# Performance work log

Hardware: AMD Instinct MI355X
Metric: run time of the kernel (lower is better)

## Reference

```python
import jax, jax.numpy as jnp
import numpy as np

B, H, E, V = 128, 1024, 1024, 40000
L, S, A = 256, 10, 10
L_S, L_A = 1.0, 1.0  # s_copy_lambda / a_copy_lambda
NEG = -1e24


def setup_inputs():
    key = jax.random.key(0)
    ks = jax.random.split(key, 32)
    n = lambda i, shape: jax.random.normal(ks[i], shape, dtype=jnp.float32)
    p = lambda i, shape: jax.random.normal(ks[i], shape, dtype=jnp.float32) * 0.02
    rnn_in = 3 * E + H  # embed + history ctx (H) + state ctx (E) + action ctx (E)
    return {
        "inp": n(0, (B, 1, E)),
        "hidden": n(1, (1, B, H)),
        "hs_vectors": n(2, (B, L, H)),
        "state_gumbel_prob": jax.random.uniform(ks[3], (B, S, V), dtype=jnp.float32),
        "state_gumbel_embed": n(4, (B, S, E)),
        "action_gumbel_prob": jax.random.uniform(ks[5], (B, A, V), dtype=jnp.float32),
        "action_gumbel_embed": n(6, (B, A, E)),
        "history_lens": jax.random.randint(ks[7], (B,), 1, L + 1),
        "history_word_indices": jax.random.randint(ks[8], (B, L), 0, V),
        # history word mlp-attention
        "Wq_hist": p(9, (H, H)), "bq_hist": jnp.zeros((H,), jnp.float32),
        "Wm_hist": p(10, (H, H)), "v_hist": p(11, (H,)),
        # init_s_attn / init_a_attn (query H, memory E)
        "Wq_s": p(12, (H, H)), "bq_s": jnp.zeros((H,), jnp.float32),
        "Wm_s": p(13, (E, H)), "v_s": p(14, (H,)),
        "Wq_a": p(15, (H, H)), "bq_a": jnp.zeros((H,), jnp.float32),
        "Wm_a": p(16, (E, H)), "v_a": p(17, (H,)),
        # sparse_copy_attn (memory E+1)
        "Wq_sc": p(18, (H, H)), "bq_sc": jnp.zeros((H,), jnp.float32),
        "Wm_sc": p(19, (E + 1, H)), "v_sc": p(20, (H,)),
        # GRU (torch layout: [3H, in], gate order r,z,n)
        "W_ih": p(21, (3 * H, rnn_in)), "W_hh": p(22, (3 * H, H)),
        "b_ih": jnp.zeros((3 * H,), jnp.float32), "b_hh": jnp.zeros((3 * H,), jnp.float32),
        # output projection
        "W_out": p(23, (H, V)), "b_out": jnp.zeros((V,), jnp.float32),
    }


def _mlp_scores(q, mem, Wq, bq, Wm, v):
    # q: [B,1,H], mem: [B,L,M] -> additive-attention logits [B,1,L]
    t = jnp.tanh((q @ Wq + bq) + (mem @ Wm))  # [B,L,H]
    return (t @ v)[:, None, :]


def reference(inp, hidden, hs_vectors, state_gumbel_prob, state_gumbel_embed,
              action_gumbel_prob, action_gumbel_embed, history_lens,
              history_word_indices, Wq_hist, bq_hist, Wm_hist, v_hist,
              Wq_s, bq_s, Wm_s, v_s, Wq_a, bq_a, Wm_a, v_a,
              Wq_sc, bq_sc, Wm_sc, v_sc, W_ih, W_hh, b_ih, b_hh, W_out, b_out):
    q0 = jnp.transpose(hidden, (1, 0, 2))  # [B,1,H]
    # --- history word attention (masked mlp attention) ---
    hist_scores = _mlp_scores(q0, hs_vectors, Wq_hist, bq_hist, Wm_hist, v_hist)
    valid = jnp.arange(L)[None, None, :] < history_lens[:, None, None]
    hist_scores = jnp.where(valid, hist_scores, NEG)
    c_his = jax.nn.softmax(hist_scores, axis=-1) @ hs_vectors  # [B,1,H]
    # --- init_consult over state / action gumbel embeddings ---
    sw = jax.nn.softmax(_mlp_scores(q0, state_gumbel_embed, Wq_s, bq_s, Wm_s, v_s), axis=-1)
    c_state = sw @ state_gumbel_embed  # [B,1,E]
    aw = jax.nn.softmax(_mlp_scores(q0, action_gumbel_embed, Wq_a, bq_a, Wm_a, v_a), axis=-1)
    c_action = aw @ action_gumbel_embed  # [B,1,E]
    x = jnp.concatenate([inp, c_his, c_state, c_action], axis=-1)[:, 0, :]  # [B,3E+H]
    # --- single-step GRU cell (torch semantics, gate order r,z,n) ---
    h0 = hidden[0]
    gi = x @ W_ih.T + b_ih
    gh = h0 @ W_hh.T + b_hh
    ir, iz, inn = jnp.split(gi, 3, axis=-1)
    hr, hz, hn = jnp.split(gh, 3, axis=-1)
    r = jax.nn.sigmoid(ir + hr)
    z = jax.nn.sigmoid(iz + hz)
    nact = jnp.tanh(inn + r * hn)
    h_new = (1.0 - z) * nact + z * h0  # [B,H]
    # --- vocab logits + copy logits, joint softmax ---
    gene_logits = h_new @ W_out + b_out  # [B,V]
    cq = h_new[:, None, :]
    hs_logits = jnp.einsum('bqh,blh->bql', cq, hs_vectors)[:, 0, :]  # dot attn, [B,L]
    s_tag = jnp.zeros((B, S, 1), jnp.float32)
    a_tag = jnp.ones((B, A, 1), jnp.float32)
    st_logits = _mlp_scores(cq, jnp.concatenate([state_gumbel_embed, s_tag], -1), Wq_sc, bq_sc, Wm_sc, v_sc)[:, 0, :]
    ac_logits = _mlp_scores(cq, jnp.concatenate([action_gumbel_embed, a_tag], -1), Wq_sc, bq_sc, Wm_sc, v_sc)[:, 0, :]
    all_logits = jnp.concatenate([gene_logits, hs_logits, st_logits, ac_logits], axis=-1)
    wp = jax.nn.softmax(all_logits, axis=-1)  # [B, V+L+S+A]
    gene_p = wp[:, :V]
    hs_w = wp[:, V:V + L]
    st_w = wp[:, V + L:V + L + S]
    ac_w = wp[:, V + L + S:]
    # --- copy-distribution mixing ---
    scp = jnp.einsum('bs,bsv->bv', st_w, state_gumbel_prob)
    acp = jnp.einsum('ba,bav->bv', ac_w, action_gumbel_prob)
    gene_p = gene_p + L_S * scp + L_A * acp
    copy_p = jnp.zeros((B, V), jnp.float32).at[jnp.arange(B)[:, None], history_word_indices].add(hs_w)
    out = jnp.log(gene_p + copy_p)[:, None, :]  # [B,1,V]
    return out, h_new[None]
```

## Files before the change

### kernel.cpp

```cpp
#include <hip/hip_runtime.h>
#include <stdint.h>

typedef __attribute__((ext_vector_type(4))) float f32x4;
typedef __attribute__((ext_vector_type(2))) unsigned int u32x2;
typedef __attribute__((ext_vector_type(4))) unsigned int u32x4;
typedef __attribute__((ext_vector_type(8))) short bf16x8;

#define BV (128*40000)

__device__ __forceinline__ unsigned rne_bf16(float f) {
    unsigned x = __float_as_uint(f);
    return ((x + 0x7FFFu + ((x >> 16) & 1u)) >> 16) & 0xFFFFu;
}
__device__ __forceinline__ unsigned pack2(float a, float b) {
    return rne_bf16(a) | (rne_bf16(b) << 16);
}
__device__ __forceinline__ float bf2f(unsigned u) {
    return __uint_as_float((u & 0xFFFFu) << 16);
}
__device__ __forceinline__ float sigm(float x) { return 1.0f / (1.0f + expf(-x)); }
__device__ __forceinline__ float ftanh(float x) {
    float e = __expf(2.0f * x);
    return 1.0f - 2.0f / (e + 1.0f);
}

__device__ __forceinline__ void gload16(const void* g, void* l) {
    __builtin_amdgcn_global_load_lds(
        (const __attribute__((address_space(1))) unsigned*)g,
        (__attribute__((address_space(3))) unsigned*)l, 16, 0, 0);
}

struct BigArgs {
    const unsigned short *hs, *WmhT, *se, *ae, *WmsT, *WmaT;
    const int* lens;
    const float *qh_h, *bq_h, *v_h;
    const float *qh_s, *bq_s, *v_s;
    const float *qh_a, *bq_a, *v_a;
    float *hsc, *stsc, *acsc;
};

__global__ __launch_bounds__(512, 1) void k_big(BigArgs a, int* __restrict__ ctr) {
    __shared__ unsigned short As[2][16384];
    __shared__ unsigned short Bs[2][16384];
    __shared__ int sTile;

    const int t = threadIdx.x, lane = t & 63, wv = t >> 6;
    const int l16 = lane & 15, lq = lane >> 4;
    const int wm = wv >> 2, wn = wv & 3;

    const int srowL = t >> 3;
    const int gccA = ((t & 7) ^ (srowL & 7)) << 3;
    const int sw = l16 & 7;
    const int c0 = ((lq ^ sw) << 3);
    const int A0 = (wm << 13) + (l16 << 6);
    const int B0 = ((wn >> 1) << 13) + ((((wn & 1) << 6) + l16) << 6);

#define STAGE(kt, d)                                                          \
    {                                                                         \
        const unsigned short* ga_ = gA + (size_t)(kt) * 64;                   \
        const unsigned short* gb_ = gB + (size_t)(kt) * 64;                   \
        _Pragma("unroll")                                                     \
        for (int h_ = 0; h_ < 2; ++h_) {                                      \
            _Pragma("unroll")                                                 \
            for (int r_ = 0; r_ < 2; ++r_) {                                  \
                size_t go_ = (size_t)(h_ * 128 + r_ * 64) * 1024;             \
                int lo_ = h_ * 8192 + r_ * 4096 + (wv << 9);                  \
                gload16(ga_ + go_, &As[d][lo_]);                              \
                gload16(gb_ + go_, &Bs[d][lo_]);                              \
            }                                                                 \
        }                                                                     \
    }

    for (;;) {
        __syncthreads();
        if (t == 0) sTile = atomicAdd(ctr, 1);
        __syncthreads();
        const int wg = sTile;
        if (wg >= 552) return;

        const unsigned short *A, *Bt;
        const float *rb, *cb, *vv;
        float* out;
        int m0, n0, vrows, rpb;
        if (wg < 40) {
            int op = wg / 20, r = wg - op * 20;
            int mt = r >> 2, nt = r & 3;
            if (op == 0) { A = a.se; Bt = a.WmsT; rb = a.qh_s; cb = a.bq_s; vv = a.v_s; out = a.stsc; }
            else         { A = a.ae; Bt = a.WmaT; rb = a.qh_a; cb = a.bq_a; vv = a.v_a; out = a.acsc; }
            m0 = mt << 8; n0 = nt << 8; vrows = 256; rpb = 10;
        } else {
            int h = wg - 40;
            int m = h >> 2, n = h & 3;
            A = a.hs; Bt = a.WmhT; rb = a.qh_h; cb = a.bq_h; vv = a.v_h; out = a.hsc;
            m0 = m << 8; n0 = n << 8; vrows = a.lens[m]; rpb = 256;
        }

        const unsigned short* gA = A + (size_t)(m0 + srowL) * 1024 + gccA;
        const unsigned short* gB = Bt + (size_t)(n0 + srowL) * 1024 + gccA;

        f32x4 acc[8][4];
#pragma unroll
        for (int i = 0; i < 8; ++i)
#pragma unroll
            for (int j = 0; j < 4; ++j) acc[i][j] = (f32x4){0.f, 0.f, 0.f, 0.f};

        STAGE(0, 0);
        for (int kt = 0; kt < 16; ++kt) {
            int cur = kt & 1;
            if (kt < 15) {
                STAGE(kt + 1, cur ^ 1);
                asm volatile("s_waitcnt vmcnt(8)" ::: "memory");
            } else {
                asm volatile("s_waitcnt vmcnt(0)" ::: "memory");
            }
            __builtin_amdgcn_s_barrier();
            __builtin_amdgcn_sched_barrier(0);

            const unsigned short* ab = As[cur];
            const unsigned short* bb = Bs[cur];
            if (vrows > (wm << 7)) {
                bf16x8 bf0[4], bf1[4];
#pragma unroll
                for (int nf = 0; nf < 4; ++nf) {
                    bf0[nf] = *(const bf16x8*)(bb + B0 + (nf << 10) + c0);
                    bf1[nf] = *(const bf16x8*)(bb + B0 + (nf << 10) + (c0 ^ 32));
                }
#pragma unroll
                for (int mf = 0; mf < 8; ++mf) {
                    if ((wm << 7) + (mf << 4) < vrows) {
                        bf16x8 a0 = *(const bf16x8*)(ab + A0 + (mf << 10) + c0);
                        bf16x8 a1 = *(const bf16x8*)(ab + A0 + (mf << 10) + (c0 ^ 32));
#pragma unroll
                        for (int nf = 0; nf < 4; ++nf)
                            acc[mf][nf] = __builtin_amdgcn_mfma_f32_16x16x32_bf16(a0, bf0[nf], acc[mf][nf], 0, 0, 0);
#pragma unroll
                        for (int nf = 0; nf < 4; ++nf)
                            acc[mf][nf] = __builtin_amdgcn_mfma_f32_16x16x32_bf16(a1, bf1[nf], acc[mf][nf], 0, 0, 0);
                    }
                }
            }
            __builtin_amdgcn_sched_barrier(0);
            __builtin_amdgcn_s_barrier();
        }

        float cbv[4], vvv[4];
        int gcs[4];
#pragma unroll
        for (int nf = 0; nf < 4; ++nf) {
            int gc = n0 + (wn << 6) + (nf << 4) + l16;
            gcs[nf] = gc; cbv[nf] = cb[gc]; vvv[nf] = vv[gc];
        }
#pragma unroll
        for (int mf = 0; mf < 8; ++mf) {
            int rloc = (wm << 7) + (mf << 4);
            if (rloc < vrows) {
#pragma unroll
                for (int r = 0; r < 4; ++r) {
                    int gr = m0 + rloc + (lq << 2) + r;
                    const float* rbp = rb + (size_t)(gr / rpb) * 1024;
                    float s = 0.f;
#pragma unroll
                    for (int nf = 0; nf < 4; ++nf) {
                        float x = acc[mf][nf][r] + rbp[gcs[nf]] + cbv[nf];
                        s += ftanh(x) * vvv[nf];
                    }
#pragma unroll
                    for (int m2 = 1; m2 < 16; m2 <<= 1) s += __shfl_xor(s, m2, 64);
                    if (l16 == 0) atomicAdd(&out[gr], s);
                }
            }
        }
    }
#undef STAGE
}

template<int EPI>
__device__ __forceinline__ void mgemm(
    const unsigned short* __restrict__ A, const unsigned short* __restrict__ Bt,
    float* __restrict__ out, const float* __restrict__ rb,
    const float* __restrict__ cb1, const float* __restrict__ cb2,
    const float* __restrict__ vvec,
    int m0, int n0, int kb, int ke, int ldk, int ldc, int rpb)
{
    __shared__ unsigned short As[2][4096];
    __shared__ unsigned short Bs[2][4096];
    const int t = threadIdx.x, lane = t & 63, wv = t >> 6;
    const int l16 = lane & 15, lq = lane >> 4;
    const int wm = wv >> 1, wn = wv & 1;

    const int srow = lane >> 2, scol = (lane & 3) << 3;
    const unsigned short* gA0 = A + (size_t)(m0 + (wv << 4) + srow) * ldk + kb + scol;
    const unsigned short* gA1 = gA0 + (size_t)64 * ldk;
    const unsigned short* gB0 = Bt + (size_t)(n0 + (wv << 4) + srow) * ldk + kb + scol;
    const unsigned short* gB1 = gB0 + (size_t)64 * ldk;
    unsigned short* lA0 = &As[0][wv << 9];
    unsigned short* lA1 = &As[0][(wv + 4) << 9];
    unsigned short* lB0 = &Bs[0][wv << 9];
    unsigned short* lB1 = &Bs[0][(wv + 4) << 9];

    f32x4 acc[4][4];
#pragma unroll
    for (int i = 0; i < 4; ++i)
#pragma unroll
        for (int j = 0; j < 4; ++j) acc[i][j] = (f32x4){0.f, 0.f, 0.f, 0.f};

    const int NS = (ke - kb) >> 5;
    gload16(gA0, lA0); gload16(gA1, lA1);
    gload16(gB0, lB0); gload16(gB1, lB1);

    for (int s = 0; s < NS; ++s) {
        __syncthreads();
        if (s + 1 < NS) {
            const int nb = (s + 1) & 1, ko = (s + 1) << 5;
            gload16(gA0 + ko, lA0 + (nb << 12)); gload16(gA1 + ko, lA1 + (nb << 12));
            gload16(gB0 + ko, lB0 + (nb << 12)); gload16(gB1 + ko, lB1 + (nb << 12));
        }
        const unsigned short* ab = As[s & 1];
        const unsigned short* bb = Bs[s & 1];
        bf16x8 af[4], bfv[4];
#pragma unroll
        for (int i = 0; i < 4; ++i)
            af[i] = *(const bf16x8*)(ab + (((wm << 6) + (i << 4) + l16) << 5) + (lq << 3));
#pragma unroll
        for (int i = 0; i < 4; ++i)
            bfv[i] = *(const bf16x8*)(bb + (((wn << 6) + (i << 4) + l16) << 5) + (lq << 3));
#pragma unroll
        for (int mf = 0; mf < 4; ++mf)
#pragma unroll
            for (int nf = 0; nf < 4; ++nf)
                acc[mf][nf] = __builtin_amdgcn_mfma_f32_16x16x32_bf16(af[mf], bfv[nf], acc[mf][nf], 0, 0, 0);
    }

    if (EPI == 1) {
#pragma unroll
        for (int mf = 0; mf < 4; ++mf) {
#pragma unroll
            for (int r = 0; r < 4; ++r) {
                int gr = m0 + (wm << 6) + (mf << 4) + (lq << 2) + r;
                const float* rbp = rb + (size_t)(gr / rpb) * 1024;
                float s = 0.0f;
#pragma unroll
                for (int nf = 0; nf < 4; ++nf) {
                    int gc = n0 + (wn << 6) + (nf << 4) + l16;
                    float xv = acc[mf][nf][r] + rbp[gc] + cb1[gc];
                    if (cb2) xv += cb2[gc];
                    s += ftanh(xv) * vvec[gc];
                }
#pragma unroll
                for (int msk = 1; msk < 16; msk <<= 1) s += __shfl_xor(s, msk, 64);
                if (l16 == 0) atomicAdd(&out[gr], s);
            }
        }
    } else {
#pragma unroll
        for (int mf = 0; mf < 4; ++mf) {
            int gr0 = m0 + (wm << 6) + (mf << 4) + (lq << 2);
#pragma unroll
            for (int nf = 0; nf < 4; ++nf) {
                int gc = n0 + (wn << 6) + (nf << 4) + l16;
#pragma unroll
                for (int r = 0; r < 4; ++r)
                    atomicAdd(&out[(size_t)(gr0 + r) * ldc + gc], acc[mf][nf][r]);
            }
        }
    }
}

__device__ __forceinline__ void gene_body(
    const unsigned short* __restrict__ hnb, const float* __restrict__ Wout,
    const float* __restrict__ b_out, float* __restrict__ out, int n0)
{
    __shared__ unsigned short As[2][4096];
    __shared__ unsigned short Bs[2][4096];
    const int t = threadIdx.x, lane = t & 63, wv = t >> 6;
    const int l16 = lane & 15, lq = lane >> 4;
    const int wm = wv >> 1, wn = wv & 1;

    const int srow = lane >> 2, scol = (lane & 3) << 3;
    const unsigned short* gA0 = hnb + (size_t)((wv << 4) + srow) * 1024 + scol;
    const unsigned short* gA1 = gA0 + (size_t)64 * 1024;
    unsigned short* lA0 = &As[0][wv << 9];
    unsigned short* lA1 = &As[0][(wv + 4) << 9];

    const int bn = t & 127, kh = t >> 7;
    const bool ok = (n0 + bn) < 40000;
    const float* gB = Wout + (size_t)(kh * 16) * 40000 + (n0 + bn);

    f32x4 acc[4][4];
#pragma unroll
    for (int i = 0; i < 4; ++i)
#pragma unroll
        for (int j = 0; j < 4; ++j) acc[i][j] = (f32x4){0.f, 0.f, 0.f, 0.f};

    auto stageB = [&](int buf, int ko) {
        const float* src = gB + (size_t)ko * 40000;
        float f[16];
#pragma unroll
        for (int j = 0; j < 16; ++j) f[j] = ok ? src[(size_t)j * 40000] : 0.0f;
        u32x4* d = (u32x4*)&Bs[buf][bn * 32 + kh * 16];
        d[0] = (u32x4){pack2(f[0],f[1]), pack2(f[2],f[3]), pack2(f[4],f[5]), pack2(f[6],f[7])};
        d[1] = (u32x4){pack2(f[8],f[9]), pack2(f[10],f[11]), pack2(f[12],f[13]), pack2(f[14],f[15])};
    };

    gload16(gA0, lA0); gload16(gA1, lA1); stageB(0, 0);
    for (int s = 0; s < 32; ++s) {
        __syncthreads();
        if (s + 1 < 32) {
            const int nb = (s + 1) & 1, ko = (s + 1) << 5;
            gload16(gA0 + ko, lA0 + (nb << 12)); gload16(gA1 + ko, lA1 + (nb << 12));
            stageB(nb, ko);
        }
        const unsigned short* ab = As[s & 1];
        const unsigned short* bb = Bs[s & 1];
        bf16x8 af[4], bfv[4];
#pragma unroll
        for (int i = 0; i < 4; ++i)
            af[i] = *(const bf16x8*)(ab + (((wm << 6) + (i << 4) + l16) << 5) + (lq << 3));
#pragma unroll
        for (int i = 0; i < 4; ++i)
            bfv[i] = *(const bf16x8*)(bb + (((wn << 6) + (i << 4) + l16) << 5) + (lq << 3));
#pragma unroll
        for (int mf = 0; mf < 4; ++mf)
#pragma unroll
            for (int nf = 0; nf < 4; ++nf)
                acc[mf][nf] = __builtin_amdgcn_mfma_f32_16x16x32_bf16(af[mf], bfv[nf], acc[mf][nf], 0, 0, 0);
    }
#pragma unroll
    for (int mf = 0; mf < 4; ++mf) {
        int gr0 = (wm << 6) + (mf << 4) + (lq << 2);
#pragma unroll
        for (int nf = 0; nf < 4; ++nf) {
            int gc = n0 + (wn << 6) + (nf << 4) + l16;
            if (gc < 40000) {
                float bo = b_out[gc];
#pragma unroll
                for (int r = 0; r < 4; ++r)
                    out[(size_t)(gr0 + r) * 40000 + gc] = acc[mf][nf][r] + bo;
            }
        }
    }
}

__global__ __launch_bounds__(256) void k_stac3(
    const unsigned short* se, const unsigned short* ae, const unsigned short* WmscT,
    const float* tagrow, const float* qsc, const float* bq_sc, const float* v_sc,
    float* stlg, float* aclg) {
    if (blockIdx.z == 0)
        mgemm<1>(se, WmscT, stlg, qsc, bq_sc, nullptr, v_sc, blockIdx.y * 128, blockIdx.x * 128, 0, 1024, 1024, 0, 10);
    else
        mgemm<1>(ae, WmscT, aclg, qsc, bq_sc, tagrow, v_sc, blockIdx.y * 128, blockIdx.x * 128, 0, 1024, 1024, 0, 10);
}

__global__ __launch_bounds__(256) void k_qh4(
    const unsigned short* q0, const unsigned short* W0, const unsigned short* W1,
    const unsigned short* W2, float* o0, float* o1, float* o2) {
    const unsigned short* W = W0; float* o = o0;
    if (blockIdx.z == 1) { W = W1; o = o1; }
    if (blockIdx.z == 2) { W = W2; o = o2; }
    int kb = blockIdx.y << 8;
    mgemm<2>(q0, W, o, nullptr, nullptr, nullptr, nullptr, 0, blockIdx.x * 128, kb, kb + 256, 1024, 1024, 1);
}

__global__ __launch_bounds__(256) void k_gigh2(
    const unsigned short* xb, const unsigned short* q0,
    const unsigned short* Wih, const unsigned short* Whh, float* gi, float* gh) {
    if (blockIdx.z == 0) {
        int kb = blockIdx.y << 9;
        mgemm<2>(xb, Wih, gi, nullptr, nullptr, nullptr, nullptr, 0, blockIdx.x * 128, kb, kb + 512, 4096, 3072, 1);
    } else {
        if (blockIdx.y >= 2) return;
        int kb = blockIdx.y << 9;
        mgemm<2>(q0, Whh, gh, nullptr, nullptr, nullptr, nullptr, 0, blockIdx.x * 128, kb, kb + 512, 1024, 3072, 1);
    }
}

__global__ __launch_bounds__(256) void k_qsc_gene(
    const unsigned short* hnb, const unsigned short* WqscT, float* qsc,
    const float* Wout, const float* b_out, float* out) {
    int id = blockIdx.x;
    if (id < 16) {
        int x = id & 7, kb = (id >> 3) << 9;
        mgemm<2>(hnb, WqscT, qsc, nullptr, nullptr, nullptr, nullptr, 0, x * 128, kb, kb + 512, 1024, 1024, 1);
    } else {
        gene_body(hnb, Wout, b_out, out, (id - 16) << 7);
    }
}

struct CvtArgs { const float* s[6]; unsigned short* d[6]; int pre[7]; };
__global__ __launch_bounds__(256) void k_cvt_all(CvtArgs a) {
    int total = a.pre[6];
    for (int i = blockIdx.x * 256 + threadIdx.x; i < total; i += gridDim.x * 256) {
        int seg = 0;
        while (i >= a.pre[seg + 1]) ++seg;
        int loc = i - a.pre[seg];
        const f32x4* s4 = (const f32x4*)a.s[seg] + (size_t)loc * 2;
        f32x4 q0 = s4[0], q1 = s4[1];
        ((u32x4*)a.d[seg])[loc] =
            (u32x4){pack2(q0[0],q0[1]), pack2(q0[2],q0[3]), pack2(q1[0],q1[1]), pack2(q1[2],q1[3])};
    }
}

struct TrArgs { const float* s[8]; unsigned short* d[8]; };
__global__ __launch_bounds__(256) void k_trcvt(TrArgs a) {
    __shared__ float tile[64][65];
    const float* in = a.s[blockIdx.z];
    unsigned short* ot = a.d[blockIdx.z];
    int k0 = blockIdx.y << 6, n0 = blockIdx.x << 6;
    int tr = threadIdx.x >> 6, tc = threadIdx.x & 63;
#pragma unroll
    for (int i = 0; i < 16; ++i) {
        int r = (i << 2) + tr;
        tile[r][tc] = in[(size_t)(k0 + r) * 1024 + n0 + tc];
    }
    __syncthreads();
#pragma unroll
    for (int i = 0; i < 16; ++i) {
        int r = (i << 2) + tr;
        ot[(size_t)(n0 + r) * 1024 + k0 + tc] = (unsigned short)rne_bf16(tile[tc][r]);
    }
}

__device__ __forceinline__ void softmax10(const float* src, float* dst) {
    float m = src[0];
    for (int i = 1; i < 10; ++i) m = fmaxf(m, src[i]);
    float z = 0.f, e[10];
    for (int i = 0; i < 10; ++i) { e[i] = expf(src[i] - m); z += e[i]; }
    float iz = 1.0f / z;
    for (int i = 0; i < 10; ++i) dst[i] = e[i] * iz;
}

__global__ __launch_bounds__(256) void k_ctx(
    const float* __restrict__ scores, const int* __restrict__ lens,
    const unsigned short* __restrict__ hs,
    const float* __restrict__ inp, const float* __restrict__ st_sc, const float* __restrict__ ac_sc,
    const unsigned short* __restrict__ se, const unsigned short* __restrict__ ae,
    unsigned short* __restrict__ xb) {
    int b = blockIdx.x, t = threadIdx.x;
    __shared__ float w[256];
    __shared__ float red[256];
    __shared__ float sw[10], aw[10];
    int len = lens[b];
    float s = scores[b * 256 + t];
    bool valid = t < len;
    red[t] = valid ? s : -3.0e38f;
    __syncthreads();
    for (int st = 128; st > 0; st >>= 1) { if (t < st) red[t] = fmaxf(red[t], red[t + st]); __syncthreads(); }
    float m = red[0];
    __syncthreads();
    float e = valid ? expf(s - m) : 0.0f;
    red[t] = e;
    __syncthreads();
    for (int st = 128; st > 0; st >>= 1) { if (t < st) red[t] += red[t + st]; __syncthreads(); }
    float Z = red[0];
    __syncthreads();
    w[t] = e / Z;
    if (t == 0) softmax10(st_sc + b * 10, sw);
    if (t == 64) softmax10(ac_sc + b * 10, aw);
    f32x4 iv = ((const f32x4*)(inp + (size_t)b * 1024))[t];
    *((u32x2*)(xb + (size_t)b * 4096) + t) = (u32x2){pack2(iv[0], iv[1]), pack2(iv[2], iv[3])};
    __syncthreads();
    float a0 = 0.f, a1 = 0.f, a2 = 0.f, a3 = 0.f;
    for (int l = 0; l < 256; ++l) {
        float wl = w[l];
        if (wl == 0.0f) continue;
        u32x2 u = *((const u32x2*)(hs + ((size_t)b * 256 + l) * 1024) + t);
        a0 += wl * bf2f(u[0]); a1 += wl * bf2f(u[0] >> 16);
        a2 += wl * bf2f(u[1]); a3 += wl * bf2f(u[1] >> 16);
    }
    *((u32x2*)(xb + (size_t)b * 4096 + 1024) + t) = (u32x2){pack2(a0, a1), pack2(a2, a3)};
    float cs0=0,cs1=0,cs2=0,cs3=0, ca0=0,ca1=0,ca2=0,ca3=0;
#pragma unroll
    for (int q = 0; q < 10; ++q) {
        u32x2 us = *((const u32x2*)(se + ((size_t)b * 10 + q) * 1024) + t);
        u32x2 ua = *((const u32x2*)(ae + ((size_t)b * 10 + q) * 1024) + t);
        float ws = sw[q], wa = aw[q];
        cs0 += ws * bf2f(us[0]); cs1 += ws * bf2f(us[0] >> 16);
        cs2 += ws * bf2f(us[1]); cs3 += ws * bf2f(us[1] >> 16);
        ca0 += wa * bf2f(ua[0]); ca1 += wa * bf2f(ua[0] >> 16);
        ca2 += wa * bf2f(ua[1]); ca3 += wa * bf2f(ua[1] >> 16);
    }
    *((u32x2*)(xb + (size_t)b * 4096 + 2048) + t) = (u32x2){pack2(cs0, cs1), pack2(cs2, cs3)};
    *((u32x2*)(xb + (size_t)b * 4096 + 3072) + t) = (u32x2){pack2(ca0, ca1), pack2(ca2, ca3)};
}

__global__ __launch_bounds__(1024) void k_gruhsl(
    const float* __restrict__ gi, const float* __restrict__ gh,
    const float* __restrict__ b_ih, const float* __restrict__ b_hh,
    const float* __restrict__ h0, float* __restrict__ hnew,
    unsigned short* __restrict__ hnb,
    const unsigned short* __restrict__ hs, float* __restrict__ hsl) {
    int b = blockIdx.x, j = threadIdx.x;
    size_t i = (size_t)b * 1024 + j;
    const float* gib = gi + (size_t)b * 3072;
    const float* ghb = gh + (size_t)b * 3072;
    float r = sigm(gib[j] + b_ih[j] + ghb[j] + b_hh[j]);
    float z = sigm(gib[1024 + j] + b_ih[1024 + j] + ghb[1024 + j] + b_hh[1024 + j]);
    float hn = ghb[2048 + j] + b_hh[2048 + j];
    float n = tanhf(gib[2048 + j] + b_ih[2048 + j] + r * hn);
    float h = (1.0f - z) * n + z * h0[i];
    hnew[i] = h;
    hnb[i] = (unsigned short)rne_bf16(h);
    __shared__ float hsm[1024];
    hsm[j] = h;
    __syncthreads();
    int wave = j >> 6, lane = j & 63;
    float hr[16];
#pragma unroll
    for (int k = 0; k < 16; ++k) hr[k] = hsm[lane * 16 + k];
    for (int l = wave; l < 256; l += 16) {
        const u32x4* row = (const u32x4*)(hs + ((size_t)b * 256 + l) * 1024);
        u32x4 u0 = row[lane * 2], u1 = row[lane * 2 + 1];
        float s = hr[0]*bf2f(u0[0]) + hr[1]*bf2f(u0[0]>>16) + hr[2]*bf2f(u0[1]) + hr[3]*bf2f(u0[1]>>16)
                + hr[4]*bf2f(u0[2]) + hr[5]*bf2f(u0[2]>>16) + hr[6]*bf2f(u0[3]) + hr[7]*bf2f(u0[3]>>16)
                + hr[8]*bf2f(u1[0]) + hr[9]*bf2f(u1[0]>>16) + hr[10]*bf2f(u1[1]) + hr[11]*bf2f(u1[1]>>16)
                + hr[12]*bf2f(u1[2]) + hr[13]*bf2f(u1[2]>>16) + hr[14]*bf2f(u1[3]) + hr[15]*bf2f(u1[3]>>16);
#pragma unroll
        for (int msk = 1; msk < 64; msk <<= 1) s += __shfl_xor(s, msk, 64);
        if (lane == 0) hsl[b * 256 + l] = s;
    }
}

__global__ __launch_bounds__(256) void k_smsc(
    const float* __restrict__ gene, const float* __restrict__ hsl,
    const float* __restrict__ stl, const float* __restrict__ acl,
    const int* __restrict__ hwi,
    float* __restrict__ mbuf, float* __restrict__ zbuf, float* __restrict__ copyp) {
    int b = blockIdx.x, t = threadIdx.x;
    __shared__ float red[256];
    const f32x4* g4 = (const f32x4*)(gene + (size_t)b * 40000);
    float mx = -3.0e38f;
    for (int i = t; i < 10000; i += 256) {
        f32x4 q = g4[i];
        mx = fmaxf(mx, fmaxf(fmaxf(q[0], q[1]), fmaxf(q[2], q[3])));
    }
    float hv = hsl[b * 256 + t];
    mx = fmaxf(mx, hv);
    if (t < 10) mx = fmaxf(mx, fmaxf(stl[b * 10 + t], acl[b * 10 + t]));
    red[t] = mx; __syncthreads();
    for (int s = 128; s > 0; s >>= 1) { if (t < s) red[t] = fmaxf(red[t], red[t + s]); __syncthreads(); }
    float m = red[0];
    __syncthreads();
    float sum = 0.f;
    for (int i = t; i < 10000; i += 256) {
        f32x4 q = g4[i];
        sum += expf(q[0]-m) + expf(q[1]-m) + expf(q[2]-m) + expf(q[3]-m);
    }
    sum += expf(hv - m);
    if (t < 10) sum += expf(stl[b * 10 + t] - m) + expf(acl[b * 10 + t] - m);
    red[t] = sum; __syncthreads();
    for (int s = 128; s > 0; s >>= 1) { if (t < s) red[t] += red[t + s]; __syncthreads(); }
    float Z = red[0];
    if (t == 0) { mbuf[b] = m; zbuf[b] = Z; }
    float wv = expf(hv - m) / Z;
    atomicAdd(copyp + (size_t)b * 40000 + hwi[b * 256 + t], wv);
}

__global__ __launch_bounds__(256) void k_final(
    float* __restrict__ gene_out, const float* __restrict__ copyp,
    const float* __restrict__ sprob, const float* __restrict__ aprob,
    const float* __restrict__ stl, const float* __restrict__ acl,
    const float* __restrict__ mbuf, const float* __restrict__ zbuf) {
    int b = blockIdx.y, t = threadIdx.x;
    __shared__ float sw[10], aw[10];
    float m = mbuf[b], iz = 1.0f / zbuf[b];
    if (t < 10) sw[t] = expf(stl[b * 10 + t] - m) * iz;
    if (t >= 64 && t < 74) aw[t - 64] = expf(acl[b * 10 + (t - 64)] - m) * iz;
    __syncthreads();
    int v4 = blockIdx.x * 256 + t;
    if (v4 < 10000) {
        size_t base = (size_t)b * 10000 + v4;
        f32x4 g = ((const f32x4*)gene_out)[base];
        f32x4 c = ((const f32x4*)copyp)[base];
        f32x4 acc;
#pragma unroll
        for (int j = 0; j < 4; ++j) acc[j] = expf(g[j] - m) * iz + c[j];
#pragma unroll
        for (int s = 0; s < 10; ++s) {
            f32x4 pv = ((const f32x4*)sprob)[((size_t)b * 10 + s) * 10000 + v4];
            f32x4 av = ((const f32x4*)aprob)[((size_t)b * 10 + s) * 10000 + v4];
            float ws = sw[s], wa = aw[s];
#pragma unroll
            for (int j = 0; j < 4; ++j) acc[j] += ws * pv[j] + wa * av[j];
        }
        f32x4 r;
#pragma unroll
        for (int j = 0; j < 4; ++j) r[j] = logf(acc[j]);
        ((f32x4*)gene_out)[base] = r;
    }
}

#define OFF_QH_H  0
#define OFF_QH_S  131072
#define OFF_QH_A  262144
#define OFF_QSC   393216
#define OFF_GI    524288
#define OFF_GH    917504
#define OFF_HSC   1310720
#define OFF_STSC  1343488
#define OFF_ACSC  1344768
#define OFF_STLG  1346048
#define OFF_ACLG  1347328
#define OFF_CTR   1348608
#define ZERO_FLOATS 1348736
#define OFF_HSL   1348736
#define OFF_M     1381504
#define OFF_Z     1381632
#define OFF_COPY  1381760
#define FLOAT_TOTAL 6501760
#define SO_HS     0
#define SO_SE     33554432
#define SO_AE     34865152
#define SO_Q0     36175872
#define SO_X      36306944
#define SO_HNB    36831232
#define SO_WQHT   36962304
#define SO_WQST   38010880
#define SO_WQAT   39059456
#define SO_WQSCT  40108032
#define SO_WMHT   41156608
#define SO_WMST   42205184
#define SO_WMAT   43253760
#define SO_WMSCT  44302336
#define SO_WIH    45350912
#define SO_WHH    57933824

extern "C" void kernel_launch(void* const* d_in, const int* in_sizes, int n_in,
                              void* d_out, int out_size, void* d_ws, size_t ws_size,
                              hipStream_t stream) {
    const float* inp     = (const float*)d_in[0];
    const float* hidden  = (const float*)d_in[1];
    const float* hs      = (const float*)d_in[2];
    const float* sprob   = (const float*)d_in[3];
    const float* se      = (const float*)d_in[4];
    const float* aprob   = (const float*)d_in[5];
    const float* ae      = (const float*)d_in[6];
    const int*   lens    = (const int*)d_in[7];
    const int*   hwi     = (const int*)d_in[8];
    const float* Wq_hist = (const float*)d_in[9];
    const float* bq_hist = (const float*)d_in[10];
    const float* Wm_hist = (const float*)d_in[11];
    const float* v_hist  = (const float*)d_in[12];
    const float* Wq_s    = (const float*)d_in[13];
    const float* bq_s    = (const float*)d_in[14];
    const float* Wm_s    = (const float*)d_in[15];
    const float* v_s     = (const float*)d_in[16];
    const float* Wq_a    = (const float*)d_in[17];
    const float* bq_a    = (const float*)d_in[18];
    const float* Wm_a    = (const float*)d_in[19];
    const float* v_a     = (const float*)d_in[20];
    const float* Wq_sc   = (const float*)d_in[21];
    const float* bq_sc   = (const float*)d_in[22];
    const float* Wm_sc   = (const float*)d_in[23];
    const float* v_sc    = (const float*)d_in[24];
    const float* W_ih    = (const float*)d_in[25];
    const float* W_hh    = (const float*)d_in[26];
    const float* b_ih    = (const float*)d_in[27];
    const float* b_hh    = (const float*)d_in[28];
    const float* W_out   = (const float*)d_in[29];
    const float* b_out   = (const float*)d_in[30];

    float* out  = (float*)d_out;
    float* w    = (float*)d_ws;
    float* hnew = out + BV;
    unsigned short* sb = (unsigned short*)(w + FLOAT_TOTAL);

    float* qh_h = w + OFF_QH_H;  float* qh_s = w + OFF_QH_S;  float* qh_a = w + OFF_QH_A;
    float* qsc  = w + OFF_QSC;   float* gi   = w + OFF_GI;    float* gh   = w + OFF_GH;
    float* hsc  = w + OFF_HSC;   float* stsc = w + OFF_STSC;  float* acsc = w + OFF_ACSC;
    float* stlg = w + OFF_STLG;  float* aclg = w + OFF_ACLG;
    float* hsl  = w + OFF_HSL;   float* mbuf = w + OFF_M;     float* zbuf = w + OFF_Z;
    float* copyp = w + OFF_COPY;
    int*   ctr  = (int*)(w + OFF_CTR);

    unsigned short* hs_bf = sb + SO_HS;   unsigned short* se_bf = sb + SO_SE;
    unsigned short* ae_bf = sb + SO_AE;   unsigned short* q0_bf = sb + SO_Q0;
    unsigned short* x_bf  = sb + SO_X;    unsigned short* hnb   = sb + SO_HNB;
    unsigned short* WqhT  = sb + SO_WQHT; unsigned short* WqsT  = sb + SO_WQST;
    unsigned short* WqaT  = sb + SO_WQAT; unsigned short* WqscT = sb + SO_WQSCT;
    unsigned short* WmhT  = sb + SO_WMHT; unsigned short* WmsT  = sb + SO_WMST;
    unsigned short* WmaT  = sb + SO_WMAT; unsigned short* WmscT = sb + SO_WMSCT;
    unsigned short* WihB  = sb + SO_WIH;  unsigned short* WhhB  = sb + SO_WHH;

    dim3 blk(256);

    hipMemsetAsync(w, 0, (size_t)ZERO_FLOATS * 4, stream);
    hipMemsetAsync(copyp, 0, (size_t)BV * 4, stream);

    CvtArgs ca;
    ca.s[0]=hs; ca.s[1]=se; ca.s[2]=ae; ca.s[3]=hidden; ca.s[4]=W_ih; ca.s[5]=W_hh;
    ca.d[0]=hs_bf; ca.d[1]=se_bf; ca.d[2]=ae_bf; ca.d[3]=q0_bf; ca.d[4]=WihB; ca.d[5]=WhhB;
    ca.pre[0]=0; ca.pre[1]=4194304; ca.pre[2]=4358144; ca.pre[3]=4521984;
    ca.pre[4]=4538368; ca.pre[5]=6111232; ca.pre[6]=6504448;
    k_cvt_all<<<dim3(4096), blk, 0, stream>>>(ca);

    TrArgs ta;
    ta.s[0]=Wq_hist; ta.s[1]=Wq_s; ta.s[2]=Wq_a; ta.s[3]=Wq_sc;
    ta.s[4]=Wm_hist; ta.s[5]=Wm_s; ta.s[6]=Wm_a; ta.s[7]=Wm_sc;
    ta.d[0]=WqhT; ta.d[1]=WqsT; ta.d[2]=WqaT; ta.d[3]=WqscT;
    ta.d[4]=WmhT; ta.d[5]=WmsT; ta.d[6]=WmaT; ta.d[7]=WmscT;
    k_trcvt<<<dim3(16, 16, 8), blk, 0, stream>>>(ta);

    k_qh4<<<dim3(8, 4, 3), blk, 0, stream>>>(q0_bf, WqhT, WqsT, WqaT, qh_h, qh_s, qh_a);

    BigArgs ba;
    ba.hs = hs_bf; ba.WmhT = WmhT; ba.se = se_bf; ba.ae = ae_bf;
    ba.WmsT = WmsT; ba.WmaT = WmaT; ba.lens = lens;
    ba.qh_h = qh_h; ba.bq_h = bq_hist; ba.v_h = v_hist;
    ba.qh_s = qh_s; ba.bq_s = bq_s; ba.v_s = v_s;
    ba.qh_a = qh_a; ba.bq_a = bq_a; ba.v_a = v_a;
    ba.hsc = hsc; ba.stsc = stsc; ba.acsc = acsc;
    k_big<<<dim3(256), dim3(512), 0, stream>>>(ba, ctr);

    k_ctx<<<dim3(128), blk, 0, stream>>>(hsc, lens, hs_bf, inp, stsc, acsc, se_bf, ae_bf, x_bf);
    k_gigh2<<<dim3(24, 8, 2), blk, 0, stream>>>(x_bf, q0_bf, WihB, WhhB, gi, gh);
    k_gruhsl<<<dim3(128), dim3(1024), 0, stream>>>(gi, gh, b_ih, b_hh, hidden, hnew, hnb, hs_bf, hsl);
    k_qsc_gene<<<dim3(329), blk, 0, stream>>>(hnb, WqscT, qsc, W_out, b_out, out);
    k_stac3<<<dim3(8, 10, 2), blk, 0, stream>>>(se_bf, ae_bf, WmscT, Wm_sc + (size_t)1024 * 1024,
                                                qsc, bq_sc, v_sc, stlg, aclg);
    k_smsc<<<dim3(128), blk, 0, stream>>>(out, hsl, stlg, aclg, hwi, mbuf, zbuf, copyp);
    k_final<<<dim3(40, 128), blk, 0, stream>>>(out, copyp, sprob, aprob, stlg, aclg, mbuf, zbuf);

    (void)in_sizes; (void)n_in; (void)out_size; (void)ws_size;
}
```

Baseline: 553.1 us.

## Compact valid history rows via prefix sum to skip padded attention GEMM tiles

Adds a prefix-sum kernel over history lengths and packs only the valid history rows into dense 256-row tiles, so the big additive-attention GEMM gathers rows through a per-tile row table. The tile count is computed on device, which drops the work spent on padded rows beyond each sequence length. Separately, the GRU/history-logit kernel is split over two blocks per batch row to raise parallelism, at the cost of recomputing the gate math in both blocks. Gathered row loads and an in-kernel binary search add some per-tile overhead.

```diff
diff --git a/kernel.cpp b/kernel.cpp
--- a/kernel.cpp
+++ b/kernel.cpp
@@ -30,20 +30,44 @@
         (__attribute__((address_space(3))) unsigned*)l, 16, 0, 0);
 }
 
+__global__ __launch_bounds__(128) void k_prefix(
+    const int* __restrict__ lens, int* __restrict__ prefix, int* __restrict__ nt) {
+    __shared__ int sc[128];
+    int t = threadIdx.x;
+    sc[t] = lens[t];
+    __syncthreads();
+    for (int off = 1; off < 128; off <<= 1) {
+        int x = (t >= off) ? sc[t - off] : 0;
+        __syncthreads();
+        sc[t] += x;
+        __syncthreads();
+    }
+    if (t == 0) prefix[0] = 0;
+    prefix[t + 1] = sc[t];
+    if (t == 127) {
+        int Mp = sc[127];
+        nt[0] = 40 + (((Mp + 255) >> 8) << 2);
+        nt[1] = Mp;
+    }
+}
+
 struct BigArgs {
     const unsigned short *hs, *WmhT, *se, *ae, *WmsT, *WmaT;
-    const int* lens;
     const float *qh_h, *bq_h, *v_h;
     const float *qh_s, *bq_s, *v_s;
     const float *qh_a, *bq_a, *v_a;
     float *hsc, *stsc, *acsc;
 };
 
-__global__ __launch_bounds__(512, 1) void k_big(BigArgs a, int* __restrict__ ctr) {
+__global__ __launch_bounds__(512, 1) void k_big(
+    BigArgs a, int* __restrict__ ctr, const int* __restrict__ prefix,
+    const int* __restrict__ ntp) {
     __shared__ unsigned short As[2][16384];
     __shared__ unsigned short Bs[2][16384];
     __shared__ int sTile;
-
+    __shared__ int rows_tab[256];
+
+    const int nTiles = ntp[0], Mp = ntp[1];
     const int t = threadIdx.x, lane = t & 63, wv = t >> 6;
     const int l16 = lane & 15, lq = lane >> 4;
     const int wm = wv >> 2, wn = wv & 3;
@@ -57,17 +81,11 @@
 
 #define STAGE(kt, d)                                                          \
     {                                                                         \
-        const unsigned short* ga_ = gA + (size_t)(kt) * 64;                   \
-        const unsigned short* gb_ = gB + (size_t)(kt) * 64;                   \
         _Pragma("unroll")                                                     \
-        for (int h_ = 0; h_ < 2; ++h_) {                                      \
-            _Pragma("unroll")                                                 \
-            for (int r_ = 0; r_ < 2; ++r_) {                                  \
-                size_t go_ = (size_t)(h_ * 128 + r_ * 64) * 1024;             \
-                int lo_ = h_ * 8192 + r_ * 4096 + (wv << 9);                  \
-                gload16(ga_ + go_, &As[d][lo_]);                              \
-                gload16(gb_ + go_, &Bs[d][lo_]);                              \
-            }                                                                 \
+        for (int q_ = 0; q_ < 4; ++q_) {                                      \
+            int lo_ = (q_ << 12) + (wv << 9);                                 \
+            gload16(gAr[q_] + (kt) * 64, &As[d][lo_]);                        \
+            gload16(gB + (size_t)(q_ << 16) + (kt) * 64, &Bs[d][lo_]);        \
         }                                                                     \
     }
 
@@ -76,26 +94,54 @@
         if (t == 0) sTile = atomicAdd(ctr, 1);
         __syncthreads();
         const int wg = sTile;
-        if (wg >= 552) return;
-
-        const unsigned short *A, *Bt;
+        if (wg >= nTiles) return;
+
+        const unsigned short *Abase, *Bt;
         const float *rb, *cb, *vv;
         float* out;
-        int m0, n0, vrows, rpb;
+        int m0, n0, vrows;
+        bool hist;
         if (wg < 40) {
+            hist = false;
             int op = wg / 20, r = wg - op * 20;
-            int mt = r >> 2, nt = r & 3;
-            if (op == 0) { A = a.se; Bt = a.WmsT; rb = a.qh_s; cb = a.bq_s; vv = a.v_s; out = a.stsc; }
-            else         { A = a.ae; Bt = a.WmaT; rb = a.qh_a; cb = a.bq_a; vv = a.v_a; out = a.acsc; }
-            m0 = mt << 8; n0 = nt << 8; vrows = 256; rpb = 10;
+            int mt = r >> 2, nt2 = r & 3;
+            if (op == 0) { Abase = a.se; Bt = a.WmsT; rb = a.qh_s; cb = a.bq_s; vv = a.v_s; out = a.stsc; }
+            else         { Abase = a.ae; Bt = a.WmaT; rb = a.qh_a; cb = a.bq_a; vv = a.v_a; out = a.acsc; }
+            m0 = mt << 8; n0 = nt2 << 8; vrows = 256;
         } else {
+            hist = true;
             int h = wg - 40;
             int m = h >> 2, n = h & 3;
-            A = a.hs; Bt = a.WmhT; rb = a.qh_h; cb = a.bq_h; vv = a.v_h; out = a.hsc;
-            m0 = m << 8; n0 = n << 8; vrows = a.lens[m]; rpb = 256;
-        }
-
-        const unsigned short* gA = A + (size_t)(m0 + srowL) * 1024 + gccA;
+            Abase = a.hs; Bt = a.WmhT; rb = a.qh_h; cb = a.bq_h; vv = a.v_h; out = a.hsc;
+            m0 = m << 8; n0 = n << 8;
+            vrows = Mp - m0; if (vrows > 256) vrows = 256;
+        }
+
+        if (t < 256) {
+            int rid;
+            if (!hist) {
+                rid = m0 + t;
+            } else {
+                int g = m0 + t;
+                if (g < Mp) {
+                    int lo = 0, hi = 128;
+                    while (hi - lo > 1) {
+                        int mid = (lo + hi) >> 1;
+                        if (prefix[mid] <= g) lo = mid; else hi = mid;
+                    }
+                    rid = (lo << 8) + (g - prefix[lo]);
+                } else {
+                    rid = 0;
+                }
+            }
+            rows_tab[t] = rid;
+        }
+        __syncthreads();
+
+        const unsigned short* gAr[4];
+#pragma unroll
+        for (int q = 0; q < 4; ++q)
+            gAr[q] = Abase + ((size_t)rows_tab[srowL + (q << 6)] << 10) + gccA;
         const unsigned short* gB = Bt + (size_t)(n0 + srowL) * 1024 + gccA;
 
         f32x4 acc[8][4];
@@ -156,8 +202,11 @@
             if (rloc < vrows) {
 #pragma unroll
                 for (int r = 0; r < 4; ++r) {
-                    int gr = m0 + rloc + (lq << 2) + r;
-                    const float* rbp = rb + (size_t)(gr / rpb) * 1024;
+                    int lrow = rloc + (lq << 2) + r;
+                    if (lrow >= vrows) continue;
+                    int gr = m0 + lrow;
+                    int bidx = hist ? (rows_tab[lrow] >> 8) : (gr / 10);
+                    const float* rbp = rb + ((size_t)bidx << 10);
                     float s = 0.f;
 #pragma unroll
                     for (int nf = 0; nf < 4; ++nf) {
@@ -431,6 +480,7 @@
 
 __global__ __launch_bounds__(256) void k_ctx(
     const float* __restrict__ scores, const int* __restrict__ lens,
+    const int* __restrict__ prefix,
     const unsigned short* __restrict__ hs,
     const float* __restrict__ inp, const float* __restrict__ st_sc, const float* __restrict__ ac_sc,
     const unsigned short* __restrict__ se, const unsigned short* __restrict__ ae,
@@ -440,9 +490,10 @@
     __shared__ float red[256];
     __shared__ float sw[10], aw[10];
     int len = lens[b];
-    float s = scores[b * 256 + t];
+    int base = prefix[b];
     bool valid = t < len;
-    red[t] = valid ? s : -3.0e38f;
+    float s = valid ? scores[base + t] : -3.0e38f;
+    red[t] = s;
     __syncthreads();
     for (int st = 128; st > 0; st >>= 1) { if (t < st) red[t] = fmaxf(red[t], red[t + st]); __syncthreads(); }
     float m = red[0];
@@ -489,7 +540,7 @@
     const float* __restrict__ h0, float* __restrict__ hnew,
     unsigned short* __restrict__ hnb,
     const unsigned short* __restrict__ hs, float* __restrict__ hsl) {
-    int b = blockIdx.x, j = threadIdx.x;
+    int b = blockIdx.x, y = blockIdx.y, j = threadIdx.x;
     size_t i = (size_t)b * 1024 + j;
     const float* gib = gi + (size_t)b * 3072;
     const float* ghb = gh + (size_t)b * 3072;
@@ -498,8 +549,10 @@
     float hn = ghb[2048 + j] + b_hh[2048 + j];
     float n = tanhf(gib[2048 + j] + b_ih[2048 + j] + r * hn);
     float h = (1.0f - z) * n + z * h0[i];
-    hnew[i] = h;
-    hnb[i] = (unsigned short)rne_bf16(h);
+    if (y == 0) {
+        hnew[i] = h;
+        hnb[i] = (unsigned short)rne_bf16(h);
+    }
     __shared__ float hsm[1024];
     hsm[j] = h;
     __syncthreads();
@@ -507,7 +560,7 @@
     float hr[16];
 #pragma unroll
     for (int k = 0; k < 16; ++k) hr[k] = hsm[lane * 16 + k];
-    for (int l = wave; l < 256; l += 16) {
+    for (int l = (y << 7) + wave; l < (y << 7) + 128; l += 16) {
         const u32x4* row = (const u32x4*)(hs + ((size_t)b * 256 + l) * 1024);
         u32x4 u0 = row[lane * 2], u1 = row[lane * 2 + 1];
         float s = hr[0]*bf2f(u0[0]) + hr[1]*bf2f(u0[0]>>16) + hr[2]*bf2f(u0[1]) + hr[3]*bf2f(u0[1]>>16)
@@ -601,12 +654,14 @@
 #define OFF_STLG  1346048
 #define OFF_ACLG  1347328
 #define OFF_CTR   1348608
-#define ZERO_FLOATS 1348736
-#define OFF_HSL   1348736
-#define OFF_M     1381504
-#define OFF_Z     1381632
-#define OFF_COPY  1381760
-#define FLOAT_TOTAL 6501760
+#define OFF_PFX   1348736
+#define OFF_NT    1348904
+#define ZERO_FLOATS 1348936
+#define OFF_HSL   1348992
+#define OFF_M     1381760
+#define OFF_Z     1381888
+#define OFF_COPY  1382016
+#define FLOAT_TOTAL 6502016
 #define SO_HS     0
 #define SO_SE     33554432
 #define SO_AE     34865152
@@ -671,6 +726,8 @@
     float* hsl  = w + OFF_HSL;   float* mbuf = w + OFF_M;     float* zbuf = w + OFF_Z;
     float* copyp = w + OFF_COPY;
     int*   ctr  = (int*)(w + OFF_CTR);
+    int*   pfx  = (int*)(w + OFF_PFX);
+    int*   ntb  = (int*)(w + OFF_NT);
 
     unsigned short* hs_bf = sb + SO_HS;   unsigned short* se_bf = sb + SO_SE;
     unsigned short* ae_bf = sb + SO_AE;   unsigned short* q0_bf = sb + SO_Q0;
@@ -686,6 +743,8 @@
     hipMemsetAsync(w, 0, (size_t)ZERO_FLOATS * 4, stream);
     hipMemsetAsync(copyp, 0, (size_t)BV * 4, stream);
 
+    k_prefix<<<dim3(1), dim3(128), 0, stream>>>(lens, pfx, ntb);
+
     CvtArgs ca;
     ca.s[0]=hs; ca.s[1]=se; ca.s[2]=ae; ca.s[3]=hidden; ca.s[4]=W_ih; ca.s[5]=W_hh;
     ca.d[0]=hs_bf; ca.d[1]=se_bf; ca.d[2]=ae_bf; ca.d[3]=q0_bf; ca.d[4]=WihB; ca.d[5]=WhhB;
@@ -704,16 +763,16 @@
 
     BigArgs ba;
     ba.hs = hs_bf; ba.WmhT = WmhT; ba.se = se_bf; ba.ae = ae_bf;
-    ba.WmsT = WmsT; ba.WmaT = WmaT; ba.lens = lens;
+    ba.WmsT = WmsT; ba.WmaT = WmaT;
     ba.qh_h = qh_h; ba.bq_h = bq_hist; ba.v_h = v_hist;
     ba.qh_s = qh_s; ba.bq_s = bq_s; ba.v_s = v_s;
     ba.qh_a = qh_a; ba.bq_a = bq_a; ba.v_a = v_a;
     ba.hsc = hsc; ba.stsc = stsc; ba.acsc = acsc;
-    k_big<<<dim3(256), dim3(512), 0, stream>>>(ba, ctr);
-
-    k_ctx<<<dim3(128), blk, 0, stream>>>(hsc, lens, hs_bf, inp, stsc, acsc, se_bf, ae_bf, x_bf);
+    k_big<<<dim3(256), dim3(512), 0, stream>>>(ba, ctr, pfx, ntb);
+
+    k_ctx<<<dim3(128), blk, 0, stream>>>(hsc, lens, pfx, hs_bf, inp, stsc, acsc, se_bf, ae_bf, x_bf);
     k_gigh2<<<dim3(24, 8, 2), blk, 0, stream>>>(x_bf, q0_bf, WihB, WhhB, gi, gh);
-    k_gruhsl<<<dim3(128), dim3(1024), 0, stream>>>(gi, gh, b_ih, b_hh, hidden, hnew, hnb, hs_bf, hsl);
+    k_gruhsl<<<dim3(128, 2), dim3(1024), 0, stream>>>(gi, gh, b_ih, b_hh, hidden, hnew, hnb, hs_bf, hsl);
     k_qsc_gene<<<dim3(329), blk, 0, stream>>>(hnb, WqscT, qsc, W_out, b_out, out);
     k_stac3<<<dim3(8, 10, 2), blk, 0, stream>>>(se_bf, ae_bf, WmscT, Wm_sc + (size_t)1024 * 1024,
                                                 qsc, bq_sc, v_sc, stlg, aclg);
```

New measurement: 556.5 us. About the same (+0.6%).
